# Kernel tuning notes

Measured on AMD Instinct MI355X. Metric: run time of the kernel, lower is better.

The kernel has to match this reference:

```python
import jax, jax.numpy as jnp
import numpy as np

B, T, D, U = 64, 512, 64, 256


def setup_inputs() -> dict:
    key = jax.random.key(0)
    k1, k2, k3, k4 = jax.random.split(key, 4)
    s = 0.05
    return {
        "x": jax.random.normal(k1, (B, T, D), dtype=jnp.float32),
        "W": jax.random.normal(k2, (D, 4 * U), dtype=jnp.float32) * s,
        "U": jax.random.normal(k3, (U, 4 * U), dtype=jnp.float32) * s,
        "b": jnp.zeros((4 * U,), dtype=jnp.float32),
        "dense_w": jax.random.normal(k4, (U, 1), dtype=jnp.float32) * s,
        "dense_b": jnp.zeros((1,), dtype=jnp.float32),
    }


def reference(x, W, U, b, dense_w, dense_b):
    # Keras LSTM with activation='relu', recurrent_activation='sigmoid'.
    # Gate packing order: i, f, c(g), o.
    units = U.shape[0]
    # Precompute input projections for all timesteps: [T, B, 4U]
    xz = jnp.einsum("btd,dg->tbg", x, W) + b

    def step(carry, xz_t):
        h, c = carry
        z = xz_t + h @ U  # [B, 4U]
        i = jax.nn.sigmoid(z[:, :units])
        f = jax.nn.sigmoid(z[:, units:2 * units])
        g = jax.nn.relu(z[:, 2 * units:3 * units])
        o = jax.nn.sigmoid(z[:, 3 * units:])
        c_new = f * c + i * g
        h_new = o * jax.nn.relu(c_new)
        return (h_new, c_new), h_new

    bsz = x.shape[0]
    h0 = jnp.zeros((bsz, units), dtype=x.dtype)
    c0 = jnp.zeros((bsz, units), dtype=x.dtype)
    _, hs = jax.lax.scan(step, (h0, c0), xz)  # hs: [T, B, U]
    hs = jnp.transpose(hs, (1, 0, 2))  # [B, T, U]
    sigma = jnp.squeeze(hs @ dense_w + dense_b, axis=-1)  # [B, T]
    return sigma
```

## Files before the change

### kernel.cpp

```cpp
#include <hip/hip_runtime.h>

#define B_  64
#define T_  512
#define D_  64
#define U_  256
#define G4  1024
#define NT  512

typedef _Float16 f16x8 __attribute__((ext_vector_type(8)));
typedef float    f32x4 __attribute__((ext_vector_type(4)));

__device__ __forceinline__ float sigmoidf_(float z) {
    return 1.f / (1.f + __expf(-z));
}

__device__ __forceinline__ f16x8 load_bfrag(const float* __restrict__ Um,
                                            int ntg, int kt, int gg, int li) {
    const float* p = Um + (size_t)(32 * kt + 8 * gg) * G4 + 16 * ntg + li;
    f16x8 v;
    #pragma unroll
    for (int e = 0; e < 8; ++e) v[e] = (_Float16)p[(size_t)e * G4];
    return v;
}

__global__ __launch_bounds__(256) void xz_kernel(const float* __restrict__ x,
                                                 const float* __restrict__ W,
                                                 const float* __restrict__ bias,
                                                 float* __restrict__ xz) {
    __shared__ float xt[16][D_];
    const int g    = blockIdx.x * 256 + threadIdx.x;
    const int row0 = blockIdx.y * 16;

    #pragma unroll
    for (int j = 0; j < 4; ++j) {
        int e = threadIdx.x + 256 * j;
        int r = e >> 6, d = e & 63;
        int row = row0 + r;
        int t = row >> 6, bb = row & 63;
        xt[r][d] = x[((size_t)bb * T_ + t) * D_ + d];
    }
    __syncthreads();

    float acc[16];
    #pragma unroll
    for (int r = 0; r < 16; ++r) acc[r] = 0.f;

    for (int d = 0; d < D_; ++d) {
        float wv = W[(size_t)d * G4 + g];
        #pragma unroll
        for (int r = 0; r < 16; ++r) acc[r] += xt[r][d] * wv;
    }

    float bg = bias[g];
    #pragma unroll
    for (int r = 0; r < 16; ++r)
        xz[(size_t)(row0 + r) * G4 + g] = acc[r] + bg;
}

__global__ __launch_bounds__(256) void pack_kernel(const float* __restrict__ Um,
                                                   f16x8* __restrict__ pk) {
    const int idx  = blockIdx.x * 256 + threadIdx.x;
    const int lane = idx & 63;
    const int fid  = idx >> 6;
    const int nt   = fid & 7;
    const int kt   = (fid >> 3) & 7;
    const int w    = fid >> 6;
    const int gg   = (lane >> 4) & 3;
    const int li   = lane & 15;
    pk[idx] = load_bfrag(Um, 8 * w + nt, kt, gg, li);
}


struct Smem {
    _Float16 h16[256];
    float    z[G4];
    float    pd[U_];
    f16x8    bl[8][17][64];
};

#define MMV(N, BV) acc##N = __builtin_amdgcn_mfma_f32_16x16x32_f16(av, (BV), acc##N, 0, 0, 0);
#define MMS(K, N)  { f16x8 bv = pkp[(((K) << 3) | (N)) << 6]; \
                     acc##N = __builtin_amdgcn_mfma_f32_16x16x32_f16(av, bv, acc##N, 0, 0, 0); }

#define MKLDS(KT, FB) { \
    f16x8 av = *(const f16x8*)&sm.h16[32 * (KT) + 8 * gg]; \
    { f16x8 bv = sm.bl[w][(FB)+0][lane]; MMV(0, bv) } \
    { f16x8 bv = sm.bl[w][(FB)+1][lane]; MMV(1, bv) } \
    { f16x8 bv = sm.bl[w][(FB)+2][lane]; MMV(2, bv) } \
    { f16x8 bv = sm.bl[w][(FB)+3][lane]; MMV(3, bv) } \
    { f16x8 bv = sm.bl[w][(FB)+4][lane]; MMV(4, bv) } \
    { f16x8 bv = sm.bl[w][(FB)+5][lane]; MMV(5, bv) } \
    { f16x8 bv = sm.bl[w][(FB)+6][lane]; MMV(6, bv) } \
    { f16x8 bv = sm.bl[w][(FB)+7][lane]; MMV(7, bv) } }

#define MKSTRM(KT) { \
    f16x8 av = *(const f16x8*)&sm.h16[32 * (KT) + 8 * gg]; \
    MMS(KT,0) MMS(KT,1) MMS(KT,2) MMS(KT,3) \
    MMS(KT,4) MMS(KT,5) MMS(KT,6) MMS(KT,7) }

__global__
__attribute__((amdgpu_flat_work_group_size(NT, NT), amdgpu_waves_per_eu(2, 2)))
void lstm_kernel(
        const float* __restrict__ Um,
        const float* __restrict__ dw,
        const float* __restrict__ dbp,
        const float* __restrict__ xz,
        const f16x8* __restrict__ pk,
        float* __restrict__ out) {
    __shared__ Smem sm;

    const int tau  = threadIdx.x;
    const int b    = blockIdx.x;
    const int w    = tau >> 6;
    const int lane = tau & 63;
    const int gg   = (tau >> 4) & 3;
    const int li   = tau & 15;
    const int w8   = 8 * w;

    const f16x8* __restrict__ pkp = pk + (((size_t)w << 6) << 6) + lane;

    #pragma unroll
    for (int f = 0; f < 17; ++f) {
        const int kt = f >> 3, nt = f & 7;
        sm.bl[w][f][lane] = load_bfrag(Um, w8 + nt, kt, gg, li);
    }

    if (tau < U_) sm.h16[tau] = (_Float16)0.f;

    const float dwr = (tau < U_) ? dw[tau] : 0.f;
    const float db0 = dbp[0];
    float c_state = 0.f;

    float xq0 = 0.f, xq1 = 0.f, xq2 = 0.f, xq3 = 0.f;
    if (tau < U_) {
        const float* xp = xz + (size_t)b * G4;
        xq0 = xp[tau]; xq1 = xp[U_ + tau]; xq2 = xp[2 * U_ + tau]; xq3 = xp[3 * U_ + tau];
    }
    __syncthreads();

    for (int t = 0; t < T_; ++t) {
        const int tn = (t + 1 < T_) ? t + 1 : t;
        float xn0 = 0.f, xn1 = 0.f, xn2 = 0.f, xn3 = 0.f;
        if (tau < U_) {
            const float* xp = xz + ((size_t)tn * B_ + b) * G4;
            xn0 = xp[tau];
            xn1 = xp[U_ + tau];
            xn2 = xp[2 * U_ + tau];
            xn3 = xp[3 * U_ + tau];
        }

        f32x4 acc0 = {0.f,0.f,0.f,0.f}, acc1 = {0.f,0.f,0.f,0.f};
        f32x4 acc2 = {0.f,0.f,0.f,0.f}, acc3 = {0.f,0.f,0.f,0.f};
        f32x4 acc4 = {0.f,0.f,0.f,0.f}, acc5 = {0.f,0.f,0.f,0.f};
        f32x4 acc6 = {0.f,0.f,0.f,0.f}, acc7 = {0.f,0.f,0.f,0.f};

        MKLDS(0, 0)
        MKLDS(1, 8)
        {
            f16x8 av = *(const f16x8*)&sm.h16[64 + 8 * gg];
            { f16x8 bv = sm.bl[w][16][lane]; MMV(0, bv) }
            MMS(2,1) MMS(2,2) MMS(2,3) MMS(2,4) MMS(2,5) MMS(2,6) MMS(2,7)
        }
        MKSTRM(3) MKSTRM(4) MKSTRM(5) MKSTRM(6) MKSTRM(7)

        if (lane < 16) {
            const int zb = 128 * w + lane;
            sm.z[zb]       = acc0.x;  sm.z[zb + 16]  = acc1.x;
            sm.z[zb + 32]  = acc2.x;  sm.z[zb + 48]  = acc3.x;
            sm.z[zb + 64]  = acc4.x;  sm.z[zb + 80]  = acc5.x;
            sm.z[zb + 96]  = acc6.x;  sm.z[zb + 112] = acc7.x;
        }
        __syncthreads();

        if (tau < U_) {
            float zi = sm.z[tau]            + xq0;
            float zf = sm.z[U_ + tau]       + xq1;
            float zg = sm.z[2 * U_ + tau]   + xq2;
            float zo = sm.z[3 * U_ + tau]   + xq3;
            float ig = sigmoidf_(zi);
            float fg = sigmoidf_(zf);
            float gv = fmaxf(zg, 0.f);
            float og = sigmoidf_(zo);
            c_state = fg * c_state + ig * gv;
            float h = og * fmaxf(c_state, 0.f);
            sm.h16[tau] = (_Float16)h;
            sm.pd[tau]  = h * dwr;
        }
        __syncthreads();

        if (tau < 64) {
            float s = sm.pd[tau] + sm.pd[tau + 64] + sm.pd[tau + 128] + sm.pd[tau + 192];
            #pragma unroll
            for (int off = 32; off > 0; off >>= 1)
                s += __shfl_down(s, off);
            if (tau == 0) out[(size_t)b * T_ + t] = s + db0;
        }

        xq0 = xn0; xq1 = xn1; xq2 = xn2; xq3 = xn3;
    }
}

#define FOR_AG(X) \
    X(2,1) X(2,2) X(2,3) X(2,4) X(2,5) X(2,6) X(2,7) \
    X(3,0) X(3,1) X(3,2) X(3,3) X(3,4) X(3,5) X(3,6) X(3,7) \
    X(4,0) X(4,1) X(4,2) X(4,3) X(4,4) X(4,5) X(4,6) X(4,7) \
    X(5,0) X(5,1) X(5,2) X(5,3) X(5,4) X(5,5) X(5,6) X(5,7) \
    X(6,0) X(6,1) X(6,2) X(6,3) X(6,4) X(6,5) X(6,6) X(6,7) \
    X(7,0) X(7,1) X(7,2) X(7,3) X(7,4) X(7,5) X(7,6) X(7,7)

#define DB(K,N) f16x8 bF_##K##_##N;
#define IB(K,N) bF_##K##_##N = load_bfrag(Um, w8 + (N), (K), gg, li);
#define MMR(K, N)  acc##N = __builtin_amdgcn_mfma_f32_16x16x32_f16(av, bF_##K##_##N, acc##N, 0, 0, 0);
#define MKREG(KT) { \
    f16x8 av = *(const f16x8*)&sm.h16[32 * (KT) + 8 * gg]; \
    MMR(KT,0) MMR(KT,1) MMR(KT,2) MMR(KT,3) \
    MMR(KT,4) MMR(KT,5) MMR(KT,6) MMR(KT,7) }

__global__
__attribute__((amdgpu_flat_work_group_size(NT, NT), amdgpu_waves_per_eu(2, 2)))
void lstm_kernel_r15(
        const float* __restrict__ Um,
        const float* __restrict__ dw,
        const float* __restrict__ dbp,
        const float* __restrict__ xz,
        float* __restrict__ out) {
    __shared__ Smem sm;

    const int tau  = threadIdx.x;
    const int b    = blockIdx.x;
    const int w    = tau >> 6;
    const int lane = tau & 63;
    const int gg   = (tau >> 4) & 3;
    const int li   = tau & 15;
    const int w8   = 8 * w;

    FOR_AG(DB)
    FOR_AG(IB)
    __builtin_amdgcn_sched_barrier(0);

    #pragma unroll
    for (int f = 0; f < 17; ++f) {
        const int kt = f >> 3, nt = f & 7;
        sm.bl[w][f][lane] = load_bfrag(Um, w8 + nt, kt, gg, li);
    }

    if (tau < U_) sm.h16[tau] = (_Float16)0.f;

    const float dwr = (tau < U_) ? dw[tau] : 0.f;
    const float db0 = dbp[0];
    float c_state = 0.f;

    float xq0 = 0.f, xq1 = 0.f, xq2 = 0.f, xq3 = 0.f;
    if (tau < U_) {
        const float* xp = xz + (size_t)b * G4;
        xq0 = xp[tau]; xq1 = xp[U_ + tau]; xq2 = xp[2 * U_ + tau]; xq3 = xp[3 * U_ + tau];
    }
    __syncthreads();

    for (int t = 0; t < T_; ++t) {
        const int tn = (t + 1 < T_) ? t + 1 : t;
        float xn0 = 0.f, xn1 = 0.f, xn2 = 0.f, xn3 = 0.f;
        if (tau < U_) {
            const float* xp = xz + ((size_t)tn * B_ + b) * G4;
            xn0 = xp[tau]; xn1 = xp[U_ + tau]; xn2 = xp[2 * U_ + tau]; xn3 = xp[3 * U_ + tau];
        }
        __builtin_amdgcn_sched_barrier(0);

        f32x4 acc0 = {0.f,0.f,0.f,0.f}, acc1 = {0.f,0.f,0.f,0.f};
        f32x4 acc2 = {0.f,0.f,0.f,0.f}, acc3 = {0.f,0.f,0.f,0.f};
        f32x4 acc4 = {0.f,0.f,0.f,0.f}, acc5 = {0.f,0.f,0.f,0.f};
        f32x4 acc6 = {0.f,0.f,0.f,0.f}, acc7 = {0.f,0.f,0.f,0.f};

        MKLDS(0, 0)
        MKLDS(1, 8)
        {
            f16x8 av = *(const f16x8*)&sm.h16[64 + 8 * gg];
            { f16x8 bv = sm.bl[w][16][lane]; MMV(0, bv) }
            MMR(2,1) MMR(2,2) MMR(2,3) MMR(2,4) MMR(2,5) MMR(2,6) MMR(2,7)
        }
        MKREG(3) MKREG(4) MKREG(5) MKREG(6) MKREG(7)

        if (lane < 16) {
            const int zb = 128 * w + lane;
            sm.z[zb]       = acc0.x;  sm.z[zb + 16]  = acc1.x;
            sm.z[zb + 32]  = acc2.x;  sm.z[zb + 48]  = acc3.x;
            sm.z[zb + 64]  = acc4.x;  sm.z[zb + 80]  = acc5.x;
            sm.z[zb + 96]  = acc6.x;  sm.z[zb + 112] = acc7.x;
        }
        __syncthreads();

        if (tau < U_) {
            float zi = sm.z[tau]            + xq0;
            float zf = sm.z[U_ + tau]       + xq1;
            float zg = sm.z[2 * U_ + tau]   + xq2;
            float zo = sm.z[3 * U_ + tau]   + xq3;
            float ig = sigmoidf_(zi);
            float fg = sigmoidf_(zf);
            float gv = fmaxf(zg, 0.f);
            float og = sigmoidf_(zo);
            c_state = fg * c_state + ig * gv;
            float h = og * fmaxf(c_state, 0.f);
            sm.h16[tau] = (_Float16)h;
            sm.pd[tau]  = h * dwr;
        }
        __syncthreads();

        if (tau < 64) {
            float s = sm.pd[tau] + sm.pd[tau + 64] + sm.pd[tau + 128] + sm.pd[tau + 192];
            #pragma unroll
            for (int off = 32; off > 0; off >>= 1)
                s += __shfl_down(s, off);
            if (tau == 0) out[(size_t)b * T_ + t] = s + db0;
        }

        xq0 = xn0; xq1 = xn1; xq2 = xn2; xq3 = xn3;
    }
}

__global__ __launch_bounds__(1024) void lstm_fallback(
        const float* __restrict__ x,  const float* __restrict__ W,
        const float* __restrict__ Um, const float* __restrict__ bias,
        const float* __restrict__ dw, const float* __restrict__ dbp,
        float* __restrict__ out) {
    __shared__ float h_s[U_];
    __shared__ float z_s2[G4];
    __shared__ float pd_s2[U_];
    const int g = threadIdx.x;
    const int b = blockIdx.x;
    const float bg  = bias[g];
    const float dwr = (g < U_) ? dw[g] : 0.f;
    const float db0 = dbp[0];
    float c = 0.f;
    if (g < U_) h_s[g] = 0.f;
    __syncthreads();
    const float* Ucol = Um + g;
    for (int t = 0; t < T_; ++t) {
        float acc = bg;
        const float* xrow = x + ((size_t)b * T_ + t) * D_;
        for (int d = 0; d < D_; ++d) acc += xrow[d] * W[(size_t)d * G4 + g];
        for (int k = 0; k < U_; ++k) acc += h_s[k] * Ucol[(size_t)k * G4];
        z_s2[g] = acc;
        __syncthreads();
        if (g < U_) {
            float ig = sigmoidf_(z_s2[g]);
            float fg = sigmoidf_(z_s2[U_ + g]);
            float gg2 = fmaxf(z_s2[2 * U_ + g], 0.f);
            float og = sigmoidf_(z_s2[3 * U_ + g]);
            c = fg * c + ig * gg2;
            float h = og * fmaxf(c, 0.f);
            h_s[g] = h; pd_s2[g] = h * dwr;
        }
        __syncthreads();
        if (g < 64) {
            float s = pd_s2[g] + pd_s2[g + 64] + pd_s2[g + 128] + pd_s2[g + 192];
            #pragma unroll
            for (int off = 32; off > 0; off >>= 1) s += __shfl_down(s, off);
            if (g == 0) out[(size_t)b * T_ + t] = s + db0;
        }
        __syncthreads();
    }
}

extern "C" void kernel_launch(void* const* d_in, const int* in_sizes, int n_in,
                              void* d_out, int out_size, void* d_ws, size_t ws_size,
                              hipStream_t stream) {
    const float* x    = (const float*)d_in[0];
    const float* W    = (const float*)d_in[1];
    const float* Um   = (const float*)d_in[2];
    const float* bias = (const float*)d_in[3];
    const float* dw   = (const float*)d_in[4];
    const float* db   = (const float*)d_in[5];
    float* out = (float*)d_out;

    const size_t need_xz = (size_t)T_ * B_ * G4 * sizeof(float);
    const size_t pk_bytes = (size_t)512 * 64 * 16;

    if (ws_size >= need_xz + pk_bytes) {
        f16x8* pk = (f16x8*)d_ws;
        float* xz = (float*)((char*)d_ws + pk_bytes);
        dim3 gridX(G4 / 256, (T_ * B_) / 16);
        xz_kernel<<<gridX, 256, 0, stream>>>(x, W, bias, xz);
        pack_kernel<<<128, 256, 0, stream>>>(Um, pk);
        lstm_kernel<<<B_, NT, 0, stream>>>(Um, dw, db, xz, pk, out);
    } else if (ws_size >= need_xz) {
        float* xz = (float*)d_ws;
        dim3 gridX(G4 / 256, (T_ * B_) / 16);
        xz_kernel<<<gridX, 256, 0, stream>>>(x, W, bias, xz);
        lstm_kernel_r15<<<B_, NT, 0, stream>>>(Um, dw, db, xz, out);
    } else {
        lstm_fallback<<<B_, 1024, 0, stream>>>(x, W, Um, bias, dw, db, out);
    }
}
```

Measured before the change: 877.1 us.

## Remap gate columns per wave so each wave computes its own units in-register

Permutes the packed recurrent-weight column tiles so each wave owns the i/f/g/o gate columns for the same 32 hidden units. The gate nonlinearities and cell update then run directly on the MFMA accumulators, which removes the shared-memory z round-trip and one barrier per timestep. The h vector and the dense partials are double-buffered, and the output reduction for step t-1 is deferred into step t, leaving a single __syncthreads per step. In exchange, the xz prefetch for the next step is dropped, so xz is loaded at the start of each step, and only half the lanes of each wave do the elementwise work.

```diff
diff --git a/kernel.cpp b/kernel.cpp
--- a/kernel.cpp
+++ b/kernel.cpp
@@ -22,6 +22,8 @@
     for (int e = 0; e < 8; ++e) v[e] = (_Float16)p[(size_t)e * G4];
     return v;
 }
+
+#define NTGW(W, NL) (16 * ((NL) >> 1) + 2 * (W) + ((NL) & 1))
 
 __global__ __launch_bounds__(256) void xz_kernel(const float* __restrict__ x,
                                                  const float* __restrict__ W,
@@ -62,27 +64,161 @@
     const int idx  = blockIdx.x * 256 + threadIdx.x;
     const int lane = idx & 63;
     const int fid  = idx >> 6;
-    const int nt   = fid & 7;
+    const int nl   = fid & 7;
     const int kt   = (fid >> 3) & 7;
     const int w    = fid >> 6;
     const int gg   = (lane >> 4) & 3;
     const int li   = lane & 15;
-    pk[idx] = load_bfrag(Um, 8 * w + nt, kt, gg, li);
-}
-
-
-struct Smem {
+    pk[idx] = load_bfrag(Um, NTGW(w, nl), kt, gg, li);
+}
+
+
+struct SmemWL {
+    _Float16 h16[2][256];
+    float    pd[2][U_];
+    f16x8    bl[8][17][64];
+};
+
+#define MMV(N, BV) acc##N = __builtin_amdgcn_mfma_f32_16x16x32_f16(av, (BV), acc##N, 0, 0, 0);
+#define MMS(K, N)  { f16x8 bv = pkp[(((K) << 3) | (N)) << 6]; \
+                     acc##N = __builtin_amdgcn_mfma_f32_16x16x32_f16(av, bv, acc##N, 0, 0, 0); }
+
+#define MKLDS(KT, FB) { \
+    f16x8 av = *(const f16x8*)&hp[32 * (KT) + 8 * gg]; \
+    { f16x8 bv = sm.bl[w][(FB)+0][lane]; MMV(0, bv) } \
+    { f16x8 bv = sm.bl[w][(FB)+1][lane]; MMV(1, bv) } \
+    { f16x8 bv = sm.bl[w][(FB)+2][lane]; MMV(2, bv) } \
+    { f16x8 bv = sm.bl[w][(FB)+3][lane]; MMV(3, bv) } \
+    { f16x8 bv = sm.bl[w][(FB)+4][lane]; MMV(4, bv) } \
+    { f16x8 bv = sm.bl[w][(FB)+5][lane]; MMV(5, bv) } \
+    { f16x8 bv = sm.bl[w][(FB)+6][lane]; MMV(6, bv) } \
+    { f16x8 bv = sm.bl[w][(FB)+7][lane]; MMV(7, bv) } }
+
+#define MKSTRM(KT) { \
+    f16x8 av = *(const f16x8*)&hp[32 * (KT) + 8 * gg]; \
+    MMS(KT,0) MMS(KT,1) MMS(KT,2) MMS(KT,3) \
+    MMS(KT,4) MMS(KT,5) MMS(KT,6) MMS(KT,7) }
+
+__global__
+__attribute__((amdgpu_flat_work_group_size(NT, NT), amdgpu_waves_per_eu(2, 2)))
+void lstm_kernel(
+        const float* __restrict__ Um,
+        const float* __restrict__ dw,
+        const float* __restrict__ dbp,
+        const float* __restrict__ xz,
+        const f16x8* __restrict__ pk,
+        float* __restrict__ out) {
+    __shared__ SmemWL sm;
+
+    const int tau  = threadIdx.x;
+    const int b    = blockIdx.x;
+    const int w    = tau >> 6;
+    const int lane = tau & 63;
+    const int gg   = (tau >> 4) & 3;
+    const int li   = tau & 15;
+    const int sel  = (lane >> 4) & 1;
+    const int u    = 32 * w + 16 * sel + li;
+
+    const f16x8* __restrict__ pkp = pk + ((size_t)w << 12) + lane;
+
+    #pragma unroll
+    for (int f = 0; f < 17; ++f) {
+        const int kt = (f < 8) ? 0 : (f < 16) ? 1 : 2;
+        const int nl = (f < 16) ? (f & 7) : (f - 16);
+        sm.bl[w][f][lane] = load_bfrag(Um, NTGW(w, nl), kt, gg, li);
+    }
+
+    if (tau < U_) sm.h16[0][tau] = (_Float16)0.f;
+
+    const float dwr = (lane < 32) ? dw[u] : 0.f;
+    const float db0 = dbp[0];
+    float c_state = 0.f;
+
+    __syncthreads();
+
+    for (int t = 0; t < T_; ++t) {
+        const int cur = t & 1, nxt = cur ^ 1;
+
+        if (t > 0 && tau < 64) {
+            const float* pp = sm.pd[nxt];
+            float s = pp[tau] + pp[tau + 64] + pp[tau + 128] + pp[tau + 192];
+            #pragma unroll
+            for (int off = 32; off > 0; off >>= 1)
+                s += __shfl_down(s, off);
+            if (tau == 0) out[(size_t)b * T_ + (t - 1)] = s + db0;
+        }
+
+        float xq0 = 0.f, xq1 = 0.f, xq2 = 0.f, xq3 = 0.f;
+        if (lane < 32) {
+            const float* xp = xz + ((size_t)t * B_ + b) * G4;
+            xq0 = xp[u];
+            xq1 = xp[256 + u];
+            xq2 = xp[512 + u];
+            xq3 = xp[768 + u];
+        }
+        __builtin_amdgcn_sched_barrier(0);
+
+        const _Float16* hp = &sm.h16[cur][0];
+        f32x4 acc0 = {0.f,0.f,0.f,0.f}, acc1 = {0.f,0.f,0.f,0.f};
+        f32x4 acc2 = {0.f,0.f,0.f,0.f}, acc3 = {0.f,0.f,0.f,0.f};
+        f32x4 acc4 = {0.f,0.f,0.f,0.f}, acc5 = {0.f,0.f,0.f,0.f};
+        f32x4 acc6 = {0.f,0.f,0.f,0.f}, acc7 = {0.f,0.f,0.f,0.f};
+
+        MKLDS(0, 0)
+        MKLDS(1, 8)
+        {
+            f16x8 av = *(const f16x8*)&hp[64 + 8 * gg];
+            { f16x8 bv = sm.bl[w][16][lane]; MMV(0, bv) }
+            MMS(2,1) MMS(2,2) MMS(2,3) MMS(2,4) MMS(2,5) MMS(2,6) MMS(2,7)
+        }
+        MKSTRM(3) MKSTRM(4) MKSTRM(5) MKSTRM(6) MKSTRM(7)
+
+        if (lane < 32) {
+            float zi = (sel ? acc1[0] : acc0[0]) + xq0;
+            float zf = (sel ? acc3[0] : acc2[0]) + xq1;
+            float zg = (sel ? acc5[0] : acc4[0]) + xq2;
+            float zo = (sel ? acc7[0] : acc6[0]) + xq3;
+            float ig = sigmoidf_(zi);
+            float fg = sigmoidf_(zf);
+            float gv = fmaxf(zg, 0.f);
+            float og = sigmoidf_(zo);
+            c_state = fg * c_state + ig * gv;
+            float h = og * fmaxf(c_state, 0.f);
+            sm.h16[nxt][u] = (_Float16)h;
+            sm.pd[cur][u]  = h * dwr;
+        }
+        __syncthreads();
+    }
+
+    if (tau < 64) {
+        const float* pp = sm.pd[(T_ - 1) & 1];
+        float s = pp[tau] + pp[tau + 64] + pp[tau + 128] + pp[tau + 192];
+        #pragma unroll
+        for (int off = 32; off > 0; off >>= 1)
+            s += __shfl_down(s, off);
+        if (tau == 0) out[(size_t)b * T_ + (T_ - 1)] = s + db0;
+    }
+}
+
+struct Smem15 {
     _Float16 h16[256];
     float    z[G4];
     float    pd[U_];
     f16x8    bl[8][17][64];
 };
 
-#define MMV(N, BV) acc##N = __builtin_amdgcn_mfma_f32_16x16x32_f16(av, (BV), acc##N, 0, 0, 0);
-#define MMS(K, N)  { f16x8 bv = pkp[(((K) << 3) | (N)) << 6]; \
-                     acc##N = __builtin_amdgcn_mfma_f32_16x16x32_f16(av, bv, acc##N, 0, 0, 0); }
-
-#define MKLDS(KT, FB) { \
+#define FOR_AG(X) \
+    X(2,1) X(2,2) X(2,3) X(2,4) X(2,5) X(2,6) X(2,7) \
+    X(3,0) X(3,1) X(3,2) X(3,3) X(3,4) X(3,5) X(3,6) X(3,7) \
+    X(4,0) X(4,1) X(4,2) X(4,3) X(4,4) X(4,5) X(4,6) X(4,7) \
+    X(5,0) X(5,1) X(5,2) X(5,3) X(5,4) X(5,5) X(5,6) X(5,7) \
+    X(6,0) X(6,1) X(6,2) X(6,3) X(6,4) X(6,5) X(6,6) X(6,7) \
+    X(7,0) X(7,1) X(7,2) X(7,3) X(7,4) X(7,5) X(7,6) X(7,7)
+
+#define DB(K,N) f16x8 bF_##K##_##N;
+#define IB(K,N) bF_##K##_##N = load_bfrag(Um, w8 + (N), (K), gg, li);
+#define MMR(K, N)  acc##N = __builtin_amdgcn_mfma_f32_16x16x32_f16(av, bF_##K##_##N, acc##N, 0, 0, 0);
+#define MKLDS15(KT, FB) { \
     f16x8 av = *(const f16x8*)&sm.h16[32 * (KT) + 8 * gg]; \
     { f16x8 bv = sm.bl[w][(FB)+0][lane]; MMV(0, bv) } \
     { f16x8 bv = sm.bl[w][(FB)+1][lane]; MMV(1, bv) } \
@@ -92,125 +228,6 @@
     { f16x8 bv = sm.bl[w][(FB)+5][lane]; MMV(5, bv) } \
     { f16x8 bv = sm.bl[w][(FB)+6][lane]; MMV(6, bv) } \
     { f16x8 bv = sm.bl[w][(FB)+7][lane]; MMV(7, bv) } }
-
-#define MKSTRM(KT) { \
-    f16x8 av = *(const f16x8*)&sm.h16[32 * (KT) + 8 * gg]; \
-    MMS(KT,0) MMS(KT,1) MMS(KT,2) MMS(KT,3) \
-    MMS(KT,4) MMS(KT,5) MMS(KT,6) MMS(KT,7) }
-
-__global__
-__attribute__((amdgpu_flat_work_group_size(NT, NT), amdgpu_waves_per_eu(2, 2)))
-void lstm_kernel(
-        const float* __restrict__ Um,
-        const float* __restrict__ dw,
-        const float* __restrict__ dbp,
-        const float* __restrict__ xz,
-        const f16x8* __restrict__ pk,
-        float* __restrict__ out) {
-    __shared__ Smem sm;
-
-    const int tau  = threadIdx.x;
-    const int b    = blockIdx.x;
-    const int w    = tau >> 6;
-    const int lane = tau & 63;
-    const int gg   = (tau >> 4) & 3;
-    const int li   = tau & 15;
-    const int w8   = 8 * w;
-
-    const f16x8* __restrict__ pkp = pk + (((size_t)w << 6) << 6) + lane;
-
-    #pragma unroll
-    for (int f = 0; f < 17; ++f) {
-        const int kt = f >> 3, nt = f & 7;
-        sm.bl[w][f][lane] = load_bfrag(Um, w8 + nt, kt, gg, li);
-    }
-
-    if (tau < U_) sm.h16[tau] = (_Float16)0.f;
-
-    const float dwr = (tau < U_) ? dw[tau] : 0.f;
-    const float db0 = dbp[0];
-    float c_state = 0.f;
-
-    float xq0 = 0.f, xq1 = 0.f, xq2 = 0.f, xq3 = 0.f;
-    if (tau < U_) {
-        const float* xp = xz + (size_t)b * G4;
-        xq0 = xp[tau]; xq1 = xp[U_ + tau]; xq2 = xp[2 * U_ + tau]; xq3 = xp[3 * U_ + tau];
-    }
-    __syncthreads();
-
-    for (int t = 0; t < T_; ++t) {
-        const int tn = (t + 1 < T_) ? t + 1 : t;
-        float xn0 = 0.f, xn1 = 0.f, xn2 = 0.f, xn3 = 0.f;
-        if (tau < U_) {
-            const float* xp = xz + ((size_t)tn * B_ + b) * G4;
-            xn0 = xp[tau];
-            xn1 = xp[U_ + tau];
-            xn2 = xp[2 * U_ + tau];
-            xn3 = xp[3 * U_ + tau];
-        }
-
-        f32x4 acc0 = {0.f,0.f,0.f,0.f}, acc1 = {0.f,0.f,0.f,0.f};
-        f32x4 acc2 = {0.f,0.f,0.f,0.f}, acc3 = {0.f,0.f,0.f,0.f};
-        f32x4 acc4 = {0.f,0.f,0.f,0.f}, acc5 = {0.f,0.f,0.f,0.f};
-        f32x4 acc6 = {0.f,0.f,0.f,0.f}, acc7 = {0.f,0.f,0.f,0.f};
-
-        MKLDS(0, 0)
-        MKLDS(1, 8)
-        {
-            f16x8 av = *(const f16x8*)&sm.h16[64 + 8 * gg];
-            { f16x8 bv = sm.bl[w][16][lane]; MMV(0, bv) }
-            MMS(2,1) MMS(2,2) MMS(2,3) MMS(2,4) MMS(2,5) MMS(2,6) MMS(2,7)
-        }
-        MKSTRM(3) MKSTRM(4) MKSTRM(5) MKSTRM(6) MKSTRM(7)
-
-        if (lane < 16) {
-            const int zb = 128 * w + lane;
-            sm.z[zb]       = acc0.x;  sm.z[zb + 16]  = acc1.x;
-            sm.z[zb + 32]  = acc2.x;  sm.z[zb + 48]  = acc3.x;
-            sm.z[zb + 64]  = acc4.x;  sm.z[zb + 80]  = acc5.x;
-            sm.z[zb + 96]  = acc6.x;  sm.z[zb + 112] = acc7.x;
-        }
-        __syncthreads();
-
-        if (tau < U_) {
-            float zi = sm.z[tau]            + xq0;
-            float zf = sm.z[U_ + tau]       + xq1;
-            float zg = sm.z[2 * U_ + tau]   + xq2;
-            float zo = sm.z[3 * U_ + tau]   + xq3;
-            float ig = sigmoidf_(zi);
-            float fg = sigmoidf_(zf);
-            float gv = fmaxf(zg, 0.f);
-            float og = sigmoidf_(zo);
-            c_state = fg * c_state + ig * gv;
-            float h = og * fmaxf(c_state, 0.f);
-            sm.h16[tau] = (_Float16)h;
-            sm.pd[tau]  = h * dwr;
-        }
-        __syncthreads();
-
-        if (tau < 64) {
-            float s = sm.pd[tau] + sm.pd[tau + 64] + sm.pd[tau + 128] + sm.pd[tau + 192];
-            #pragma unroll
-            for (int off = 32; off > 0; off >>= 1)
-                s += __shfl_down(s, off);
-            if (tau == 0) out[(size_t)b * T_ + t] = s + db0;
-        }
-
-        xq0 = xn0; xq1 = xn1; xq2 = xn2; xq3 = xn3;
-    }
-}
-
-#define FOR_AG(X) \
-    X(2,1) X(2,2) X(2,3) X(2,4) X(2,5) X(2,6) X(2,7) \
-    X(3,0) X(3,1) X(3,2) X(3,3) X(3,4) X(3,5) X(3,6) X(3,7) \
-    X(4,0) X(4,1) X(4,2) X(4,3) X(4,4) X(4,5) X(4,6) X(4,7) \
-    X(5,0) X(5,1) X(5,2) X(5,3) X(5,4) X(5,5) X(5,6) X(5,7) \
-    X(6,0) X(6,1) X(6,2) X(6,3) X(6,4) X(6,5) X(6,6) X(6,7) \
-    X(7,0) X(7,1) X(7,2) X(7,3) X(7,4) X(7,5) X(7,6) X(7,7)
-
-#define DB(K,N) f16x8 bF_##K##_##N;
-#define IB(K,N) bF_##K##_##N = load_bfrag(Um, w8 + (N), (K), gg, li);
-#define MMR(K, N)  acc##N = __builtin_amdgcn_mfma_f32_16x16x32_f16(av, bF_##K##_##N, acc##N, 0, 0, 0);
 #define MKREG(KT) { \
     f16x8 av = *(const f16x8*)&sm.h16[32 * (KT) + 8 * gg]; \
     MMR(KT,0) MMR(KT,1) MMR(KT,2) MMR(KT,3) \
@@ -224,7 +241,7 @@
         const float* __restrict__ dbp,
         const float* __restrict__ xz,
         float* __restrict__ out) {
-    __shared__ Smem sm;
+    __shared__ Smem15 sm;
 
     const int tau  = threadIdx.x;
     const int b    = blockIdx.x;
@@ -271,8 +288,8 @@
         f32x4 acc4 = {0.f,0.f,0.f,0.f}, acc5 = {0.f,0.f,0.f,0.f};
         f32x4 acc6 = {0.f,0.f,0.f,0.f}, acc7 = {0.f,0.f,0.f,0.f};
 
-        MKLDS(0, 0)
-        MKLDS(1, 8)
+        MKLDS15(0, 0)
+        MKLDS15(1, 8)
         {
             f16x8 av = *(const f16x8*)&sm.h16[64 + 8 * gg];
             { f16x8 bv = sm.bl[w][16][lane]; MMV(0, bv) }
@@ -372,7 +389,7 @@
     const float* db   = (const float*)d_in[5];
     float* out = (float*)d_out;
 
-    const size_t need_xz = (size_t)T_ * B_ * G4 * sizeof(float);
+    const size_t need_xz  = (size_t)T_ * B_ * G4 * sizeof(float);
     const size_t pk_bytes = (size_t)512 * 64 * 16;
 
     if (ws_size >= need_xz + pk_bytes) {
```

After: 839.7 us. 1.04x faster.
